# Optimization experiments

Hardware: AMD Instinct MI355X
Metric: run time of the kernel (lower is better)

The kernel has to match this reference:

```python
import jax, jax.numpy as jnp
import numpy as np

EPS = 1e-12
LN_EPS = 1e-5
RIDGE = 0.01
M, L, T = 256, 4096, 2048


def setup_inputs() -> dict:
    key = jax.random.key(0)
    ks = jax.random.split(key, 16)
    inp = {
        "gamma": jax.random.uniform(ks[0], (L,), dtype=jnp.float32),
        "A_re": jax.random.normal(ks[1], (M, L), dtype=jnp.float32),
        "A_im": jax.random.normal(ks[2], (M, L), dtype=jnp.float32),
        "X_re": jax.random.normal(ks[3], (M, T), dtype=jnp.float32),
        "X_im": jax.random.normal(ks[4], (M, T), dtype=jnp.float32),
        # LayerNorm(L) params
        "ln_w": jnp.ones((L,), jnp.float32),
        "ln_b": jnp.zeros((L,), jnp.float32),
        # MultiheadAttention(embed_dim=1, num_heads=1): in_proj [3,1]->[3], out_proj [1,1]->[1]
        "in_w": jax.random.normal(ks[5], (3,), dtype=jnp.float32),
        "in_b": jnp.zeros((3,), jnp.float32),
        "out_w": jax.random.normal(ks[6], (1,), dtype=jnp.float32),
        "out_b": jnp.zeros((1,), jnp.float32),
        # gate Linear(L, L)
        "gate_W": jax.random.normal(ks[7], (L, L), dtype=jnp.float32) * (1.0 / np.sqrt(L)),
        "gate_b": jnp.zeros((L,), jnp.float32),
        # learned scalars
        "delta": jnp.float32(0.5),
        "lmbda": jnp.float32(0.01),
    }
    return inp


def _iaa_forward(gamma, A_re, A_im, X_re, X_im, ln_w, ln_b, in_w, in_b,
                 out_w, out_b, gate_W, gate_b, delta, lmbda):
    A = (A_re + 1j * A_im).astype(jnp.complex64)      # [M, L]
    X = (X_re + 1j * X_im).astype(jnp.complex64)      # [M, T]
    p = gamma                                         # [L]

    # R = A diag(p) A^H + ridge * I   (MxM)
    AP = A * p[None, :].astype(A.dtype)
    R = AP @ A.conj().T + RIDGE * jnp.eye(M, dtype=A.dtype)
    Rinv = jnp.linalg.inv(R)                          # [M, M]

    Ah = A.conj().T                                   # [L, M]
    ARi = Ah @ Rinv                                   # [L, M]
    S = ARi @ X                                       # [L, T]
    q = jnp.sum(jnp.abs(S) ** 2, axis=1)              # [L]
    d = jnp.real(jnp.sum(ARi * Ah, axis=1))           # [L]
    v = q / (d + EPS)

    # constrain_gamma -> sigmoid(delta); use_residual
    dlt = jax.nn.sigmoid(delta)
    u = p + dlt * (v - p)

    # LayerNorm over the full length-L vector
    mu = jnp.mean(u)
    var = jnp.mean((u - mu) ** 2)
    u_p = (u - mu) / jnp.sqrt(var + LN_EPS) * ln_w + ln_b

    # MultiheadAttention(embed_dim=1, num_heads=1) over seq of L tokens, scale = 1/sqrt(1) = 1
    qv = u_p * in_w[0] + in_b[0]                      # [L]
    kv = u_p * in_w[1] + in_b[1]
    vv = u_p * in_w[2] + in_b[2]
    scores = qv[:, None] * kv[None, :]                # [L, L]
    attn = jax.nn.softmax(scores, axis=-1)
    attn_out = (attn @ vv) * out_w[0] + out_b[0]      # [L]

    # gating on u (pre-layernorm), as in the torch code
    g = jax.nn.sigmoid(gate_W @ u + gate_b)           # Linear: u @ W.T + b, u is 1-D -> W @ u + b
    r = g * v + (1.0 - g) * p

    s = r + attn_out
    return jax.nn.relu(s - lmbda)


def reference(gamma, A_re, A_im, X_re, X_im, ln_w, ln_b, in_w, in_b,
              out_w, out_b, gate_W, gate_b, delta, lmbda):
    return _iaa_forward(gamma, A_re, A_im, X_re, X_im, ln_w, ln_b, in_w, in_b,
                        out_w, out_b, gate_W, gate_b, delta, lmbda)
```

## Files before the change

kernel.cpp:

```cpp
#include <hip/hip_runtime.h>
#include <hip/hip_bf16.h>
#include <math.h>

#define MM 256
#define LL 4096
#define TT 2048

typedef __attribute__((ext_vector_type(8))) short bf16x8;
typedef __attribute__((ext_vector_type(4))) float f32x4;
typedef __attribute__((ext_vector_type(4))) unsigned short us4;
typedef unsigned short ushort_t;

#define OFF_G      131072
#define OFF_Q      262144
#define OFF_D      266240
#define OFF_V      270336
#define OFF_U      274432
#define OFF_UP     278528
#define ZERO_FL    290816
#define OFF_RINVP  290816
#define OFF_GP     421888
#define OFF_APL    552960
#define OFF_XPL    2650112
#define OFF_ATP    3698688
#define OFF_WTP    5795840
#define OFF_XA     9990144
#define OFF_XB     10121216
#define OFF_EA     10252288
#define OFF_EB     10383360

#define MFMA3(ACC, AH, AL, BH, BL)                                              \
  ACC = __builtin_amdgcn_mfma_f32_16x16x32_bf16(AH, BH, ACC, 0, 0, 0);          \
  ACC = __builtin_amdgcn_mfma_f32_16x16x32_bf16(AH, BL, ACC, 0, 0, 0);          \
  ACC = __builtin_amdgcn_mfma_f32_16x16x32_bf16(AL, BH, ACC, 0, 0, 0);

__device__ __forceinline__ void split_bf16(float x, ushort_t& h, ushort_t& l) {
  __hip_bfloat16 bh = __float2bfloat16(x);
  h = *(ushort_t*)&bh;
  __hip_bfloat16 bl = __float2bfloat16(x - __bfloat162float(bh));
  l = *(ushort_t*)&bl;
}
__device__ __forceinline__ float bfu2f(ushort_t u) {
  unsigned v = ((unsigned)u) << 16;
  float f;
  __builtin_memcpy(&f, &v, 4);
  return f;
}

__device__ __forceinline__ float wave_red_sum(float v) {
#pragma unroll
  for (int o = 32; o > 0; o >>= 1) v += __shfl_down(v, o);
  return v;
}
__device__ __forceinline__ float wave_red_max(float v) {
#pragma unroll
  for (int o = 32; o > 0; o >>= 1) v = fmaxf(v, __shfl_down(v, o));
  return v;
}
__device__ float blk_red_sum(float v) {
  __shared__ float sh[4];
  int lane = threadIdx.x & 63, wv = threadIdx.x >> 6;
  v = wave_red_sum(v);
  __syncthreads();
  if (lane == 0) sh[wv] = v;
  __syncthreads();
  return sh[0] + sh[1] + sh[2] + sh[3];
}
__device__ float blk_red_max(float v) {
  __shared__ float shm[4];
  int lane = threadIdx.x & 63, wv = threadIdx.x >> 6;
  v = wave_red_max(v);
  __syncthreads();
  if (lane == 0) shm[wv] = v;
  __syncthreads();
  return fmaxf(fmaxf(shm[0], shm[1]), fmaxf(shm[2], shm[3]));
}

__device__ __forceinline__ float2 r_mirror(const float2* __restrict__ R, int i, int j) {
  if ((i >> 6) >= (j >> 6)) return R[i * 256 + j];
  float2 r = R[j * 256 + i];
  r.y = -r.y;
  return r;
}

__global__ __launch_bounds__(256) void k_prep(float* __restrict__ ws,
                                              const float* __restrict__ Are,
                                              const float* __restrict__ Aim,
                                              const float* __restrict__ Xre,
                                              const float* __restrict__ Xim,
                                              const float* __restrict__ gamma) {
  __shared__ float tr[32][33], ti[32][33];
  int bid = blockIdx.x, tid = threadIdx.x;
  if (bid < 1136) {
    int idx = bid * 256 + tid;
    float v = 0.0f;
    if (idx < 131072 && (idx % 514) == 0) v = 0.01f;
    ws[idx] = v;
  } else if (bid < 2160) {
    int i4 = (bid - 1136) * 256 + tid;
    ushort_t* dst = (ushort_t*)(ws + OFF_APL);
    float4 re = ((const float4*)Are)[i4];
    float4 im = ((const float4*)Aim)[i4];
    float4 ga = ((const float4*)gamma)[i4 & (LL / 4 - 1)];
    float sr[4] = {re.x * sqrtf(ga.x), re.y * sqrtf(ga.y), re.z * sqrtf(ga.z), re.w * sqrtf(ga.w)};
    float si[4] = {im.x * sqrtf(ga.x), im.y * sqrtf(ga.y), im.z * sqrtf(ga.z), im.w * sqrtf(ga.w)};
    us4 hr, lr, hi, li;
#pragma unroll
    for (int e = 0; e < 4; ++e) {
      ushort_t h, l;
      split_bf16(sr[e], h, l); hr[e] = h; lr[e] = l;
      split_bf16(si[e], h, l); hi[e] = h; li[e] = l;
    }
    size_t o = (size_t)i4 * 4;
    *(us4*)(dst + o) = hr;
    *(us4*)(dst + (size_t)MM * LL + o) = lr;
    *(us4*)(dst + 2 * (size_t)MM * LL + o) = hi;
    *(us4*)(dst + 3 * (size_t)MM * LL + o) = li;
  } else if (bid < 2672) {
    int i4 = (bid - 2160) * 256 + tid;
    ushort_t* dst = (ushort_t*)(ws + OFF_XPL);
    float4 re = ((const float4*)Xre)[i4];
    float4 im = ((const float4*)Xim)[i4];
    float fr[4] = {re.x, re.y, re.z, re.w};
    float fi[4] = {im.x, im.y, im.z, im.w};
    us4 hr, lr, hi, li;
#pragma unroll
    for (int e = 0; e < 4; ++e) {
      ushort_t h, l;
      split_bf16(fr[e], h, l); hr[e] = h; lr[e] = l;
      split_bf16(fi[e], h, l); hi[e] = h; li[e] = l;
    }
    size_t o = (size_t)i4 * 4;
    *(us4*)(dst + o) = hr;
    *(us4*)(dst + (size_t)MM * TT + o) = lr;
    *(us4*)(dst + 2 * (size_t)MM * TT + o) = hi;
    *(us4*)(dst + 3 * (size_t)MM * TT + o) = li;
  } else {
    int b2 = bid - 2672;
    ushort_t* dst = (ushort_t*)(ws + OFF_ATP);
    int c0 = (b2 & 127) * 32, r0 = (b2 >> 7) * 32;
    int tx = tid & 31, tg = tid >> 5;
#pragma unroll
    for (int i = 0; i < 4; ++i) {
      int r = tg + 8 * i;
      tr[r][tx] = Are[(size_t)(r0 + r) * LL + c0 + tx];
      ti[r][tx] = Aim[(size_t)(r0 + r) * LL + c0 + tx];
    }
    __syncthreads();
#pragma unroll
    for (int i = 0; i < 4; ++i) {
      int rr = tg + 8 * i;
      size_t o = (size_t)(c0 + rr) * 256 + r0 + tx;
      ushort_t h, l;
      split_bf16(tr[tx][rr], h, l);
      dst[o] = h;
      dst[o + 1048576] = l;
      split_bf16(ti[tx][rr], h, l);
      dst[o + 2097152] = h;
      dst[o + 3145728] = l;
    }
  }
}

__global__ __launch_bounds__(256, 4) void k_gram_both(float* __restrict__ ws) {
  __shared__ __align__(16) ushort_t sA[4][64][40];
  __shared__ __align__(16) ushort_t sB[4][64][40];
  const int ti_lu[10] = {0, 1, 1, 2, 2, 2, 3, 3, 3, 3};
  const int tj_lu[10] = {0, 0, 1, 0, 1, 2, 0, 1, 2, 3};
  int bid = blockIdx.x;
  const ushort_t* pl;
  float* C;
  int K, tile, ksplit;
  size_t PS;
  if (bid < 320) {
    pl = (const ushort_t*)(ws + OFF_APL);
    C = ws;
    K = LL;
    PS = (size_t)MM * LL;
    tile = bid % 10;
    ksplit = bid / 10;
  } else {
    int b2 = bid - 320;
    pl = (const ushort_t*)(ws + OFF_XPL);
    C = ws + OFF_G;
    K = TT;
    PS = (size_t)MM * TT;
    tile = b2 % 10;
    ksplit = b2 / 10;
  }
  int kbeg = ksplit * 128;
  int i0 = ti_lu[tile] * 64, j0 = tj_lu[tile] * 64;
  bool diag = (i0 == j0);
  int tid = threadIdx.x;
  int lane = tid & 63, wv = tid >> 6;
  int srow = tid >> 2, sslot = tid & 3;
  int arow = wv * 16 + (lane & 15);
  int kq = (lane >> 4) * 8;
  f32x4 z = {0.f, 0.f, 0.f, 0.f};
  f32x4 Zrr[4], Zri[4], Zir[4], Zii[4];
#pragma unroll
  for (int s = 0; s < 4; ++s) { Zrr[s] = z; Zri[s] = z; Zir[s] = z; Zii[s] = z; }

  for (int chunk = 0; chunk < 4; ++chunk) {
    int k0 = kbeg + chunk * 32;
    __syncthreads();
#pragma unroll
    for (int p = 0; p < 4; ++p) {
      *(bf16x8*)&sA[p][srow][sslot * 8] =
          *(const bf16x8*)(pl + p * PS + (size_t)(i0 + srow) * K + k0 + sslot * 8);
      if (!diag)
        *(bf16x8*)&sB[p][srow][sslot * 8] =
            *(const bf16x8*)(pl + p * PS + (size_t)(j0 + srow) * K + k0 + sslot * 8);
    }
    __syncthreads();
    bf16x8 arh = *(const bf16x8*)&sA[0][arow][kq];
    bf16x8 arl = *(const bf16x8*)&sA[1][arow][kq];
    bf16x8 aih = *(const bf16x8*)&sA[2][arow][kq];
    bf16x8 ail = *(const bf16x8*)&sA[3][arow][kq];
    ushort_t(*bs)[64][40] = diag ? sA : sB;
#pragma unroll
    for (int s = 0; s < 4; ++s) {
      int brow = s * 16 + (lane & 15);
      bf16x8 brh = *(const bf16x8*)&bs[0][brow][kq];
      bf16x8 brl = *(const bf16x8*)&bs[1][brow][kq];
      bf16x8 bih = *(const bf16x8*)&bs[2][brow][kq];
      bf16x8 bil = *(const bf16x8*)&bs[3][brow][kq];
      MFMA3(Zrr[s], arh, arl, brh, brl);
      MFMA3(Zri[s], arh, arl, bih, bil);
      MFMA3(Zir[s], aih, ail, brh, brl);
      MFMA3(Zii[s], aih, ail, bih, bil);
    }
  }
  int rbase = i0 + wv * 16 + (lane >> 4) * 4;
#pragma unroll
  for (int s = 0; s < 4; ++s) {
    int col = j0 + s * 16 + (lane & 15);
#pragma unroll
    for (int r = 0; r < 4; ++r) {
      float re = Zrr[s][r] + Zii[s][r];
      float im = Zir[s][r] - Zri[s][r];
      float* p = C + ((size_t)(rbase + r) * 256 + col) * 2;
      atomicAdd(p, re);
      atomicAdd(p + 1, im);
    }
  }
}

__global__ __launch_bounds__(256) void k_n1(float* __restrict__ ws) {
  __shared__ float2 As[16][17], Bs[16][17];
  const float2* R = (const float2*)ws;
  int bid = blockIdx.x, tid = threadIdx.x;
  if (bid < 256) {
    float2* E1 = (float2*)(ws + OFF_EA);
    int i0 = (bid >> 4) * 16, j0 = (bid & 15) * 16;
    int tx = tid & 15, ty = tid >> 4;
    int rowA = i0 + ty;
    float DiA = R[rowA * 257].x;
    float accx = 0.f, accy = 0.f;
    for (int k0 = 0; k0 < 256; k0 += 16) {
      __syncthreads();
      {
        int c = k0 + tx;
        float2 r = r_mirror(R, rowA, c);
        float dl = (rowA == c) ? 1.0f : 0.0f;
        As[ty][tx] = make_float2(dl - r.x / DiA, -r.y / DiA);
      }
      {
        int rB = k0 + ty, c = j0 + tx;
        float DiB = R[rB * 257].x;
        float2 r = r_mirror(R, rB, c);
        float dl = (rB == c) ? 1.0f : 0.0f;
        Bs[ty][tx] = make_float2(dl - r.x / DiB, -r.y / DiB);
      }
      __syncthreads();
#pragma unroll
      for (int kk = 0; kk < 16; ++kk) {
        float2 a = As[ty][kk], bb = Bs[kk][tx];
        accx += a.x * bb.x - a.y * bb.y;
        accy += a.x * bb.y + a.y * bb.x;
      }
    }
    E1[rowA * 256 + j0 + tx] = make_float2(accx, accy);
  } else if (bid < 512) {
    float2* X1 = (float2*)(ws + OFF_XA);
    int idx = (bid - 256) * 256 + tid;
    int i = idx >> 8, j = idx & 255;
    float Dii = R[i * 257].x;
    float Djj = R[j * 257].x;
    float2 r = r_mirror(R, i, j);
    float dl = (i == j) ? 1.0f : 0.0f;
    float ex = dl - r.x / Dii;
    float ey = -r.y / Dii;
    X1[idx] = make_float2((dl + ex) / Djj, ey / Djj);
  } else {
    const float2* src = (const float2*)(ws + OFF_G);
    ushort_t* dst = (ushort_t*)(ws + OFF_GP);
    int idx = (bid - 512) * 256 + tid;
    int i = idx >> 8, j = idx & 255;
    float2 v = r_mirror(src, i, j);
    ushort_t h, l;
    split_bf16(v.x, h, l);
    dst[idx] = h;
    dst[idx + 65536] = l;
    split_bf16(v.y, h, l);
    dst[idx + 131072] = h;
    dst[idx + 196608] = l;
  }
}

__global__ __launch_bounds__(256) void k_newt_step(const float2* __restrict__ Xin,
                                                   const float2* __restrict__ Ein,
                                                   float2* __restrict__ Xout,
                                                   float2* __restrict__ Eout, int xblocks) {
  __shared__ float2 As[16][17], Bs[16][17];
  int bid = blockIdx.x;
  bool isX = bid < xblocks;
  int b = isX ? bid : bid - xblocks;
  const float2* Bm = isX ? Xin : Ein;
  int i0 = (b >> 4) * 16, j0 = (b & 15) * 16;
  int tx = threadIdx.x & 15, ty = threadIdx.x >> 4;
  float accx = 0.f, accy = 0.f;
  for (int k0 = 0; k0 < 256; k0 += 16) {
    __syncthreads();
    As[ty][tx] = Ein[(i0 + ty) * 256 + k0 + tx];
    Bs[ty][tx] = Bm[(k0 + ty) * 256 + j0 + tx];
    __syncthreads();
#pragma unroll
    for (int kk = 0; kk < 16; ++kk) {
      float2 a = As[ty][kk], bb = Bs[kk][tx];
      accx += a.x * bb.x - a.y * bb.y;
      accy += a.x * bb.y + a.y * bb.x;
    }
  }
  int idx = (i0 + ty) * 256 + j0 + tx;
  if (isX) {
    float2 x = Xin[idx];
    Xout[idx] = make_float2(x.x + accx, x.y + accy);
  } else {
    Eout[idx] = make_float2(accx, accy);
  }
}

__global__ __launch_bounds__(256) void k_newt_fin(const float2* __restrict__ Xin,
                                                  const float2* __restrict__ Ein,
                                                  ushort_t* __restrict__ dst) {
  __shared__ float2 As[16][17], Bs[16][17];
  int b = blockIdx.x;
  int i0 = (b >> 4) * 16, j0 = (b & 15) * 16;
  int tx = threadIdx.x & 15, ty = threadIdx.x >> 4;
  float accx = 0.f, accy = 0.f;
  for (int k0 = 0; k0 < 256; k0 += 16) {
    __syncthreads();
    As[ty][tx] = Ein[(i0 + ty) * 256 + k0 + tx];
    Bs[ty][tx] = Xin[(k0 + ty) * 256 + j0 + tx];
    __syncthreads();
#pragma unroll
    for (int kk = 0; kk < 16; ++kk) {
      float2 a = As[ty][kk], bb = Bs[kk][tx];
      accx += a.x * bb.x - a.y * bb.y;
      accy += a.x * bb.y + a.y * bb.x;
    }
  }
  int idx = (i0 + ty) * 256 + j0 + tx;
  float2 x = Xin[idx];
  float vx = x.x + accx, vy = x.y + accy;
  ushort_t h, l;
  split_bf16(vx, h, l);
  dst[idx] = h;
  dst[idx + 65536] = l;
  split_bf16(vy, h, l);
  dst[idx + 131072] = h;
  dst[idx + 196608] = l;
}

__global__ __launch_bounds__(256) void k_wide_mfma(const ushort_t* __restrict__ Ap,
                                                   const ushort_t* __restrict__ Bp,
                                                   const float* __restrict__ AuxRe,
                                                   const float* __restrict__ AuxIm,
                                                   ushort_t* __restrict__ WTout,
                                                   float* __restrict__ dq, int mode) {
  __shared__ __align__(16) ushort_t sB[4][64][40];
  const ushort_t* arh_p = Ap;
  const ushort_t* arl_p = Ap + 65536;
  const ushort_t* aih_p = Ap + 131072;
  const ushort_t* ail_p = Ap + 196608;
  const ushort_t* brh_p = Bp;
  const ushort_t* brl_p = Bp + 1048576;
  const ushort_t* bih_p = Bp + 2097152;
  const ushort_t* bil_p = Bp + 3145728;
  int j0 = blockIdx.x * 64;
  int i0 = blockIdx.y * 64;
  int tid = threadIdx.x;
  int lane = tid & 63, wv = tid >> 6;
  int srow = tid >> 2, sslot = tid & 3;
  int m = i0 + wv * 16 + (lane & 15);
  int kq = (lane >> 4) * 8;
  f32x4 z = {0.f, 0.f, 0.f, 0.f};
  f32x4 Zrr[4], Zri[4], Zir[4], Zii[4];
#pragma unroll
  for (int s = 0; s < 4; ++s) { Zrr[s] = z; Zri[s] = z; Zir[s] = z; Zii[s] = z; }
  for (int k0 = 0; k0 < 256; k0 += 32) {
    __syncthreads();
    {
      size_t bo = (size_t)(j0 + srow) * 256 + k0 + sslot * 8;
      *(bf16x8*)&sB[0][srow][sslot * 8] = *(const bf16x8*)(brh_p + bo);
      *(bf16x8*)&sB[1][srow][sslot * 8] = *(const bf16x8*)(brl_p + bo);
      *(bf16x8*)&sB[2][srow][sslot * 8] = *(const bf16x8*)(bih_p + bo);
      *(bf16x8*)&sB[3][srow][sslot * 8] = *(const bf16x8*)(bil_p + bo);
    }
    __syncthreads();
    size_t ao = (size_t)m * 256 + k0 + kq;
    bf16x8 arh = *(const bf16x8*)(arh_p + ao);
    bf16x8 arl = *(const bf16x8*)(arl_p + ao);
    bf16x8 aih = *(const bf16x8*)(aih_p + ao);
    bf16x8 ail = *(const bf16x8*)(ail_p + ao);
#pragma unroll
    for (int s = 0; s < 4; ++s) {
      int brow = s * 16 + (lane & 15);
      bf16x8 brh = *(const bf16x8*)&sB[0][brow][kq];
      bf16x8 brl = *(const bf16x8*)&sB[1][brow][kq];
      bf16x8 bih = *(const bf16x8*)&sB[2][brow][kq];
      bf16x8 bil = *(const bf16x8*)&sB[3][brow][kq];
      MFMA3(Zrr[s], arh, arl, brh, brl);
      MFMA3(Zri[s], arh, arl, bih, bil);
      MFMA3(Zir[s], aih, ail, brh, brl);
      MFMA3(Zii[s], aih, ail, bih, bil);
    }
  }
  int rbase = i0 + wv * 16 + (lane >> 4) * 4;
#pragma unroll
  for (int s = 0; s < 4; ++s) {
    int col = j0 + s * 16 + (lane & 15);
    size_t wo = (size_t)col * 256 + rbase;
    float part = 0.f;
    if (mode == 0) {
      us4 hr, lr, hi, li;
#pragma unroll
      for (int r = 0; r < 4; ++r) {
        float re = Zrr[s][r] - Zii[s][r];
        float im = Zri[s][r] + Zir[s][r];
        ushort_t h, l;
        split_bf16(re, h, l);
        hr[r] = h; lr[r] = l;
        split_bf16(im, h, l);
        hi[r] = h; li[r] = l;
        size_t o = (size_t)(rbase + r) * LL + col;
        part += re * AuxRe[o] - im * AuxIm[o];
      }
      *(us4*)(WTout + wo) = hr;
      *(us4*)(WTout + 1048576 + wo) = lr;
      *(us4*)(WTout + 2097152 + wo) = hi;
      *(us4*)(WTout + 3145728 + wo) = li;
    } else {
      us4 wh = *(const us4*)(brh_p + wo);
      us4 wl = *(const us4*)(brl_p + wo);
      us4 wih = *(const us4*)(bih_p + wo);
      us4 wil = *(const us4*)(bil_p + wo);
#pragma unroll
      for (int r = 0; r < 4; ++r) {
        float re = Zrr[s][r] - Zii[s][r];
        float im = Zri[s][r] + Zir[s][r];
        float wx = bfu2f(wh[r]) + bfu2f(wl[r]);
        float wy = bfu2f(wih[r]) + bfu2f(wil[r]);
        part += wx * re + wy * im;
      }
    }
    part += __shfl_down(part, 32);
    part += __shfl_down(part, 16);
    if ((lane >> 4) == 0) atomicAdd(dq + col, part);
  }
}

__global__ __launch_bounds__(256) void k_uvln(float* __restrict__ ws,
                                              const float* __restrict__ gamma,
                                              const float* __restrict__ delta,
                                              const float* __restrict__ lnw,
                                              const float* __restrict__ lnb) {
  const float* q = ws + OFF_Q;
  const float* d = ws + OFF_D;
  float* vvec = ws + OFF_V;
  float* uvec = ws + OFF_U;
  float* up = ws + OFF_UP;
  int tid = threadIdx.x;
  float dlt = 1.0f / (1.0f + expf(-delta[0]));
  float s = 0.f;
  for (int i = tid; i < LL; i += 256) {
    float v = q[i] / (d[i] + 1e-12f);
    float p = gamma[i];
    float u = p + dlt * (v - p);
    vvec[i] = v;
    uvec[i] = u;
    s += u;
  }
  float mu = blk_red_sum(s) * (1.0f / LL);
  float s2 = 0.f;
  for (int i = tid; i < LL; i += 256) { float dd = uvec[i] - mu; s2 += dd * dd; }
  float var = blk_red_sum(s2) * (1.0f / LL);
  float inv = rsqrtf(var + 1e-5f);
  for (int i = tid; i < LL; i += 256) up[i] = (uvec[i] - mu) * inv * lnw[i] + lnb[i];
}

__global__ __launch_bounds__(256) void k_gateattn(const float* __restrict__ ws,
                                                  const float* __restrict__ Wg,
                                                  const float* __restrict__ gb,
                                                  const float* __restrict__ inw,
                                                  const float* __restrict__ inb,
                                                  const float* __restrict__ outw,
                                                  const float* __restrict__ outb,
                                                  const float* __restrict__ gamma,
                                                  const float* __restrict__ lmbda,
                                                  float* __restrict__ out) {
  const float* uvec = ws + OFF_U;
  const float* up = ws + OFF_UP;
  const float* vvec = ws + OFF_V;
  int i = blockIdx.x, tid = threadIdx.x;
  const float4* wr = (const float4*)(Wg + (size_t)i * LL);
  const float4* u4 = (const float4*)uvec;
  float s = 0.f;
  for (int j = tid; j < LL / 4; j += 256) {
    float4 w = wr[j], x = u4[j];
    s += w.x * x.x + w.y * x.y + w.z * x.z + w.w * x.w;
  }
  float tot = blk_red_sum(s);
  float g = 1.0f / (1.0f + expf(-(tot + gb[i])));
  float qv = up[i] * inw[0] + inb[0];
  float w1 = inw[1], b1 = inb[1], w2 = inw[2], b2 = inb[2];
  const float4* up4 = (const float4*)up;
  float mx = -3.4e38f;
  for (int j = tid; j < LL / 4; j += 256) {
    float4 u = up4[j];
    mx = fmaxf(mx, fmaxf(fmaxf(qv * (u.x * w1 + b1), qv * (u.y * w1 + b1)),
                         fmaxf(qv * (u.z * w1 + b1), qv * (u.w * w1 + b1))));
  }
  mx = blk_red_max(mx);
  float den = 0.f, num = 0.f;
  for (int j = tid; j < LL / 4; j += 256) {
    float4 u = up4[j];
    float e0 = expf(qv * (u.x * w1 + b1) - mx);
    float e1 = expf(qv * (u.y * w1 + b1) - mx);
    float e2 = expf(qv * (u.z * w1 + b1) - mx);
    float e3 = expf(qv * (u.w * w1 + b1) - mx);
    den += e0 + e1 + e2 + e3;
    num += e0 * (u.x * w2 + b2) + e1 * (u.y * w2 + b2) + e2 * (u.z * w2 + b2) + e3 * (u.w * w2 + b2);
  }
  den = blk_red_sum(den);
  num = blk_red_sum(num);
  if (tid == 0) {
    float attn = (num / den) * outw[0] + outb[0];
    float r = g * vvec[i] + (1.0f - g) * gamma[i] + attn - lmbda[0];
    out[i] = fmaxf(r, 0.0f);
  }
}

extern "C" void kernel_launch(void* const* d_in, const int* in_sizes, int n_in,
                              void* d_out, int out_size, void* d_ws, size_t ws_size,
                              hipStream_t stream) {
  const float* gamma = (const float*)d_in[0];
  const float* Are   = (const float*)d_in[1];
  const float* Aim   = (const float*)d_in[2];
  const float* Xre   = (const float*)d_in[3];
  const float* Xim   = (const float*)d_in[4];
  const float* lnw   = (const float*)d_in[5];
  const float* lnb   = (const float*)d_in[6];
  const float* inw   = (const float*)d_in[7];
  const float* inb   = (const float*)d_in[8];
  const float* outw  = (const float*)d_in[9];
  const float* outb  = (const float*)d_in[10];
  const float* gateW = (const float*)d_in[11];
  const float* gateb = (const float*)d_in[12];
  const float* delta = (const float*)d_in[13];
  const float* lmbda = (const float*)d_in[14];
  float* out = (float*)d_out;
  float* ws = (float*)d_ws;

  float2* XA = (float2*)(ws + OFF_XA);
  float2* XB = (float2*)(ws + OFF_XB);
  float2* EA = (float2*)(ws + OFF_EA);
  float2* EB = (float2*)(ws + OFF_EB);
  ushort_t* Rinvp = (ushort_t*)(ws + OFF_RINVP);

  k_prep<<<3696, 256, 0, stream>>>(ws, Are, Aim, Xre, Xim, gamma);
  k_gram_both<<<480, 256, 0, stream>>>(ws);
  k_n1<<<768, 256, 0, stream>>>(ws);
  k_newt_step<<<512, 256, 0, stream>>>(XA, EA, XB, EB, 256);
  k_newt_step<<<512, 256, 0, stream>>>(XB, EB, XA, EA, 256);
  k_newt_step<<<512, 256, 0, stream>>>(XA, EA, XB, EB, 256);
  k_newt_fin<<<256, 256, 0, stream>>>(XB, EB, Rinvp);

  k_wide_mfma<<<dim3(64, 4), 256, 0, stream>>>(Rinvp, (ushort_t*)(ws + OFF_ATP),
                                               Are, Aim, (ushort_t*)(ws + OFF_WTP),
                                               ws + OFF_D, 0);
  k_wide_mfma<<<dim3(64, 4), 256, 0, stream>>>((ushort_t*)(ws + OFF_GP),
                                               (ushort_t*)(ws + OFF_WTP),
                                               nullptr, nullptr, nullptr, ws + OFF_Q, 1);
  k_uvln<<<1, 256, 0, stream>>>(ws, gamma, delta, lnw, lnb);
  k_gateattn<<<LL, 256, 0, stream>>>(ws, gateW, gateb, inw, inb, outw, outb, gamma, lmbda, out);
}
```

Measured before the change: 308.2 us.

## Replace Gram atomics with split-K partials, last-block reduce, and fuse LN into gate kernel

The Gram kernel now writes per-split partial tiles to a workspace buffer instead of using float atomics. The last block per tile, found through an atomic counter, sums the partials, adds the ridge and writes the mirrored Hermitian R. For the X Gram, that block also writes the bf16-split G directly, so the r_mirror reads and the G packing blocks in k_n1 go away. A large zero-fill in k_prep also disappears. The single-block k_uvln kernel is removed, and every gateattn block recomputes v, u and the LayerNorm statistics redundantly, trading extra arithmetic and memory reads for one less serial launch.

```diff
diff --git a/kernel.cpp b/kernel.cpp
--- a/kernel.cpp
+++ b/kernel.cpp
@@ -11,13 +11,9 @@
 typedef __attribute__((ext_vector_type(4))) unsigned short us4;
 typedef unsigned short ushort_t;
 
-#define OFF_G      131072
 #define OFF_Q      262144
 #define OFF_D      266240
-#define OFF_V      270336
-#define OFF_U      274432
-#define OFF_UP     278528
-#define ZERO_FL    290816
+#define OFF_CNT    270336
 #define OFF_RINVP  290816
 #define OFF_GP     421888
 #define OFF_APL    552960
@@ -28,6 +24,8 @@
 #define OFF_XB     10121216
 #define OFF_EA     10252288
 #define OFF_EB     10383360
+#define OFF_PA     10514432
+#define OFF_PX     13135872
 
 #define MFMA3(ACC, AH, AL, BH, BL)                                              \
   ACC = __builtin_amdgcn_mfma_f32_16x16x32_bf16(AH, BH, ACC, 0, 0, 0);          \
@@ -76,13 +74,6 @@
   return fmaxf(fmaxf(shm[0], shm[1]), fmaxf(shm[2], shm[3]));
 }
 
-__device__ __forceinline__ float2 r_mirror(const float2* __restrict__ R, int i, int j) {
-  if ((i >> 6) >= (j >> 6)) return R[i * 256 + j];
-  float2 r = R[j * 256 + i];
-  r.y = -r.y;
-  return r;
-}
-
 __global__ __launch_bounds__(256) void k_prep(float* __restrict__ ws,
                                               const float* __restrict__ Are,
                                               const float* __restrict__ Aim,
@@ -91,13 +82,10 @@
                                               const float* __restrict__ gamma) {
   __shared__ float tr[32][33], ti[32][33];
   int bid = blockIdx.x, tid = threadIdx.x;
-  if (bid < 1136) {
-    int idx = bid * 256 + tid;
-    float v = 0.0f;
-    if (idx < 131072 && (idx % 514) == 0) v = 0.01f;
-    ws[idx] = v;
-  } else if (bid < 2160) {
-    int i4 = (bid - 1136) * 256 + tid;
+  if (bid < 33) {
+    ws[OFF_Q + bid * 256 + tid] = 0.0f;
+  } else if (bid < 1057) {
+    int i4 = (bid - 33) * 256 + tid;
     ushort_t* dst = (ushort_t*)(ws + OFF_APL);
     float4 re = ((const float4*)Are)[i4];
     float4 im = ((const float4*)Aim)[i4];
@@ -116,8 +104,8 @@
     *(us4*)(dst + (size_t)MM * LL + o) = lr;
     *(us4*)(dst + 2 * (size_t)MM * LL + o) = hi;
     *(us4*)(dst + 3 * (size_t)MM * LL + o) = li;
-  } else if (bid < 2672) {
-    int i4 = (bid - 2160) * 256 + tid;
+  } else if (bid < 1569) {
+    int i4 = (bid - 1057) * 256 + tid;
     ushort_t* dst = (ushort_t*)(ws + OFF_XPL);
     float4 re = ((const float4*)Xre)[i4];
     float4 im = ((const float4*)Xim)[i4];
@@ -136,7 +124,7 @@
     *(us4*)(dst + 2 * (size_t)MM * TT + o) = hi;
     *(us4*)(dst + 3 * (size_t)MM * TT + o) = li;
   } else {
-    int b2 = bid - 2672;
+    int b2 = bid - 1569;
     ushort_t* dst = (ushort_t*)(ws + OFF_ATP);
     int c0 = (b2 & 127) * 32, r0 = (b2 >> 7) * 32;
     int tx = tid & 31, tg = tid >> 5;
@@ -165,29 +153,18 @@
 __global__ __launch_bounds__(256, 4) void k_gram_both(float* __restrict__ ws) {
   __shared__ __align__(16) ushort_t sA[4][64][40];
   __shared__ __align__(16) ushort_t sB[4][64][40];
+  __shared__ int rflag;
   const int ti_lu[10] = {0, 1, 1, 2, 2, 2, 3, 3, 3, 3};
   const int tj_lu[10] = {0, 0, 1, 0, 1, 2, 0, 1, 2, 3};
   int bid = blockIdx.x;
-  const ushort_t* pl;
-  float* C;
-  int K, tile, ksplit;
-  size_t PS;
-  if (bid < 320) {
-    pl = (const ushort_t*)(ws + OFF_APL);
-    C = ws;
-    K = LL;
-    PS = (size_t)MM * LL;
-    tile = bid % 10;
-    ksplit = bid / 10;
-  } else {
-    int b2 = bid - 320;
-    pl = (const ushort_t*)(ws + OFF_XPL);
-    C = ws + OFF_G;
-    K = TT;
-    PS = (size_t)MM * TT;
-    tile = b2 % 10;
-    ksplit = b2 / 10;
-  }
+  bool isA = bid < 320;
+  int b2 = isA ? bid : bid - 320;
+  const ushort_t* pl = (const ushort_t*)(ws + (isA ? OFF_APL : OFF_XPL));
+  int K = isA ? LL : TT;
+  size_t PS = (size_t)MM * K;
+  int tile = b2 % 10, ksplit = b2 / 10;
+  int S = isA ? 32 : 16;
+  float2* Pbase = (float2*)(ws + (isA ? OFF_PA : OFF_PX));
   int kbeg = ksplit * 128;
   int i0 = ti_lu[tile] * 64, j0 = tj_lu[tile] * 64;
   bool diag = (i0 == j0);
@@ -231,17 +208,61 @@
       MFMA3(Zii[s], aih, ail, bih, bil);
     }
   }
-  int rbase = i0 + wv * 16 + (lane >> 4) * 4;
+  float2* Pt = Pbase + ((size_t)ksplit * 10 + tile) * 4096;
 #pragma unroll
   for (int s = 0; s < 4; ++s) {
-    int col = j0 + s * 16 + (lane & 15);
+    int lcol = s * 16 + (lane & 15);
 #pragma unroll
     for (int r = 0; r < 4; ++r) {
+      int lrow = wv * 16 + (lane >> 4) * 4 + r;
       float re = Zrr[s][r] + Zii[s][r];
       float im = Zir[s][r] - Zri[s][r];
-      float* p = C + ((size_t)(rbase + r) * 256 + col) * 2;
-      atomicAdd(p, re);
-      atomicAdd(p + 1, im);
+      Pt[lrow * 64 + lcol] = make_float2(re, im);
+    }
+  }
+  __threadfence();
+  if (tid == 0) {
+    int* cnt = (int*)(ws + OFF_CNT);
+    int old = atomicAdd(&cnt[(isA ? 0 : 10) + tile], 1);
+    rflag = (old == S - 1);
+  }
+  __syncthreads();
+  if (!rflag) return;
+  __threadfence();
+  float2* Rc = (float2*)ws;
+  ushort_t* Gp = (ushort_t*)(ws + OFF_GP);
+  int e0 = tid * 16;
+  for (int e = e0; e < e0 + 16; e += 2) {
+    float4 acc = {0.f, 0.f, 0.f, 0.f};
+    for (int s = 0; s < S; ++s) {
+      float4 v = *(const float4*)&Pbase[((size_t)s * 10 + tile) * 4096 + e];
+      acc.x += v.x; acc.y += v.y; acc.z += v.z; acc.w += v.w;
+    }
+    int li = e >> 6, lj = e & 63;
+    int gi = i0 + li, gj = j0 + lj;
+    if (isA) {
+      if (diag && gi == gj) acc.x += 0.01f;
+      if (diag && gi == gj + 1) acc.z += 0.01f;
+      Rc[gi * 256 + gj] = make_float2(acc.x, acc.y);
+      Rc[gi * 256 + gj + 1] = make_float2(acc.z, acc.w);
+      if (!diag) {
+        Rc[gj * 256 + gi] = make_float2(acc.x, -acc.y);
+        Rc[(gj + 1) * 256 + gi] = make_float2(acc.z, -acc.w);
+      }
+    } else {
+      ushort_t h, l;
+      int idx = gi * 256 + gj;
+      split_bf16(acc.x, h, l); Gp[idx] = h; Gp[idx + 65536] = l;
+      split_bf16(acc.y, h, l); Gp[idx + 131072] = h; Gp[idx + 196608] = l;
+      split_bf16(acc.z, h, l); Gp[idx + 1] = h; Gp[idx + 1 + 65536] = l;
+      split_bf16(acc.w, h, l); Gp[idx + 1 + 131072] = h; Gp[idx + 1 + 196608] = l;
+      if (!diag) {
+        int m0 = gj * 256 + gi, m1 = (gj + 1) * 256 + gi;
+        split_bf16(acc.x, h, l); Gp[m0] = h; Gp[m0 + 65536] = l;
+        split_bf16(-acc.y, h, l); Gp[m0 + 131072] = h; Gp[m0 + 196608] = l;
+        split_bf16(acc.z, h, l); Gp[m1] = h; Gp[m1 + 65536] = l;
+        split_bf16(-acc.w, h, l); Gp[m1 + 131072] = h; Gp[m1 + 196608] = l;
+      }
     }
   }
 }
@@ -261,14 +282,14 @@
       __syncthreads();
       {
         int c = k0 + tx;
-        float2 r = r_mirror(R, rowA, c);
+        float2 r = R[rowA * 256 + c];
         float dl = (rowA == c) ? 1.0f : 0.0f;
         As[ty][tx] = make_float2(dl - r.x / DiA, -r.y / DiA);
       }
       {
         int rB = k0 + ty, c = j0 + tx;
         float DiB = R[rB * 257].x;
-        float2 r = r_mirror(R, rB, c);
+        float2 r = R[rB * 256 + c];
         float dl = (rB == c) ? 1.0f : 0.0f;
         Bs[ty][tx] = make_float2(dl - r.x / DiB, -r.y / DiB);
       }
@@ -281,30 +302,17 @@
       }
     }
     E1[rowA * 256 + j0 + tx] = make_float2(accx, accy);
-  } else if (bid < 512) {
+  } else {
     float2* X1 = (float2*)(ws + OFF_XA);
     int idx = (bid - 256) * 256 + tid;
     int i = idx >> 8, j = idx & 255;
     float Dii = R[i * 257].x;
     float Djj = R[j * 257].x;
-    float2 r = r_mirror(R, i, j);
+    float2 r = R[i * 256 + j];
     float dl = (i == j) ? 1.0f : 0.0f;
     float ex = dl - r.x / Dii;
     float ey = -r.y / Dii;
     X1[idx] = make_float2((dl + ex) / Djj, ey / Djj);
-  } else {
-    const float2* src = (const float2*)(ws + OFF_G);
-    ushort_t* dst = (ushort_t*)(ws + OFF_GP);
-    int idx = (bid - 512) * 256 + tid;
-    int i = idx >> 8, j = idx & 255;
-    float2 v = r_mirror(src, i, j);
-    ushort_t h, l;
-    split_bf16(v.x, h, l);
-    dst[idx] = h;
-    dst[idx + 65536] = l;
-    split_bf16(v.y, h, l);
-    dst[idx + 131072] = h;
-    dst[idx + 196608] = l;
   }
 }
 
@@ -471,35 +479,6 @@
   }
 }
 
-__global__ __launch_bounds__(256) void k_uvln(float* __restrict__ ws,
-                                              const float* __restrict__ gamma,
-                                              const float* __restrict__ delta,
-                                              const float* __restrict__ lnw,
-                                              const float* __restrict__ lnb) {
-  const float* q = ws + OFF_Q;
-  const float* d = ws + OFF_D;
-  float* vvec = ws + OFF_V;
-  float* uvec = ws + OFF_U;
-  float* up = ws + OFF_UP;
-  int tid = threadIdx.x;
-  float dlt = 1.0f / (1.0f + expf(-delta[0]));
-  float s = 0.f;
-  for (int i = tid; i < LL; i += 256) {
-    float v = q[i] / (d[i] + 1e-12f);
-    float p = gamma[i];
-    float u = p + dlt * (v - p);
-    vvec[i] = v;
-    uvec[i] = u;
-    s += u;
-  }
-  float mu = blk_red_sum(s) * (1.0f / LL);
-  float s2 = 0.f;
-  for (int i = tid; i < LL; i += 256) { float dd = uvec[i] - mu; s2 += dd * dd; }
-  float var = blk_red_sum(s2) * (1.0f / LL);
-  float inv = rsqrtf(var + 1e-5f);
-  for (int i = tid; i < LL; i += 256) up[i] = (uvec[i] - mu) * inv * lnw[i] + lnb[i];
-}
-
 __global__ __launch_bounds__(256) void k_gateattn(const float* __restrict__ ws,
                                                   const float* __restrict__ Wg,
                                                   const float* __restrict__ gb,
@@ -508,46 +487,86 @@
                                                   const float* __restrict__ outw,
                                                   const float* __restrict__ outb,
                                                   const float* __restrict__ gamma,
+                                                  const float* __restrict__ delta,
+                                                  const float* __restrict__ lnw,
+                                                  const float* __restrict__ lnb,
                                                   const float* __restrict__ lmbda,
                                                   float* __restrict__ out) {
-  const float* uvec = ws + OFF_U;
-  const float* up = ws + OFF_UP;
-  const float* vvec = ws + OFF_V;
+  const float4* q4 = (const float4*)(ws + OFF_Q);
+  const float4* d4 = (const float4*)(ws + OFF_D);
+  const float4* g4 = (const float4*)gamma;
+  const float4* lw4 = (const float4*)lnw;
+  const float4* lb4 = (const float4*)lnb;
   int i = blockIdx.x, tid = threadIdx.x;
-  const float4* wr = (const float4*)(Wg + (size_t)i * LL);
-  const float4* u4 = (const float4*)uvec;
+  float dlt = 1.0f / (1.0f + expf(-delta[0]));
   float s = 0.f;
   for (int j = tid; j < LL / 4; j += 256) {
-    float4 w = wr[j], x = u4[j];
-    s += w.x * x.x + w.y * x.y + w.z * x.z + w.w * x.w;
-  }
-  float tot = blk_red_sum(s);
+    float4 qv = q4[j], dv = d4[j], pv = g4[j];
+    s += pv.x + dlt * (qv.x / (dv.x + 1e-12f) - pv.x);
+    s += pv.y + dlt * (qv.y / (dv.y + 1e-12f) - pv.y);
+    s += pv.z + dlt * (qv.z / (dv.z + 1e-12f) - pv.z);
+    s += pv.w + dlt * (qv.w / (dv.w + 1e-12f) - pv.w);
+  }
+  float mu = blk_red_sum(s) * (1.0f / LL);
+  float s2 = 0.f;
+  for (int j = tid; j < LL / 4; j += 256) {
+    float4 qv = q4[j], dv = d4[j], pv = g4[j];
+    float u0 = pv.x + dlt * (qv.x / (dv.x + 1e-12f) - pv.x) - mu;
+    float u1 = pv.y + dlt * (qv.y / (dv.y + 1e-12f) - pv.y) - mu;
+    float u2 = pv.z + dlt * (qv.z / (dv.z + 1e-12f) - pv.z) - mu;
+    float u3 = pv.w + dlt * (qv.w / (dv.w + 1e-12f) - pv.w) - mu;
+    s2 += u0 * u0 + u1 * u1 + u2 * u2 + u3 * u3;
+  }
+  float var = blk_red_sum(s2) * (1.0f / LL);
+  float inv = rsqrtf(var + 1e-5f);
+  const float* qs = ws + OFF_Q;
+  const float* ds = ws + OFF_D;
+  float v_i = qs[i] / (ds[i] + 1e-12f);
+  float u_i = gamma[i] + dlt * (v_i - gamma[i]);
+  float up_i = (u_i - mu) * inv * lnw[i] + lnb[i];
+  float qvv = up_i * inw[0] + inb[0];
+  float w1 = inw[1], b1 = inb[1], w2 = inw[2], b2 = inb[2];
+  const float4* wr = (const float4*)(Wg + (size_t)i * LL);
+  float sdot = 0.f, mx = -3.4e38f;
+  for (int j = tid; j < LL / 4; j += 256) {
+    float4 qv = q4[j], dv = d4[j], pv = g4[j], w = wr[j], lwv = lw4[j], lbv = lb4[j];
+    float u0 = pv.x + dlt * (qv.x / (dv.x + 1e-12f) - pv.x);
+    float u1 = pv.y + dlt * (qv.y / (dv.y + 1e-12f) - pv.y);
+    float u2 = pv.z + dlt * (qv.z / (dv.z + 1e-12f) - pv.z);
+    float u3 = pv.w + dlt * (qv.w / (dv.w + 1e-12f) - pv.w);
+    sdot += w.x * u0 + w.y * u1 + w.z * u2 + w.w * u3;
+    float k0 = ((u0 - mu) * inv * lwv.x + lbv.x) * w1 + b1;
+    float k1 = ((u1 - mu) * inv * lwv.y + lbv.y) * w1 + b1;
+    float k2 = ((u2 - mu) * inv * lwv.z + lbv.z) * w1 + b1;
+    float k3 = ((u3 - mu) * inv * lwv.w + lbv.w) * w1 + b1;
+    mx = fmaxf(mx, fmaxf(fmaxf(qvv * k0, qvv * k1), fmaxf(qvv * k2, qvv * k3)));
+  }
+  float tot = blk_red_sum(sdot);
+  mx = blk_red_max(mx);
   float g = 1.0f / (1.0f + expf(-(tot + gb[i])));
-  float qv = up[i] * inw[0] + inb[0];
-  float w1 = inw[1], b1 = inb[1], w2 = inw[2], b2 = inb[2];
-  const float4* up4 = (const float4*)up;
-  float mx = -3.4e38f;
-  for (int j = tid; j < LL / 4; j += 256) {
-    float4 u = up4[j];
-    mx = fmaxf(mx, fmaxf(fmaxf(qv * (u.x * w1 + b1), qv * (u.y * w1 + b1)),
-                         fmaxf(qv * (u.z * w1 + b1), qv * (u.w * w1 + b1))));
-  }
-  mx = blk_red_max(mx);
   float den = 0.f, num = 0.f;
   for (int j = tid; j < LL / 4; j += 256) {
-    float4 u = up4[j];
-    float e0 = expf(qv * (u.x * w1 + b1) - mx);
-    float e1 = expf(qv * (u.y * w1 + b1) - mx);
-    float e2 = expf(qv * (u.z * w1 + b1) - mx);
-    float e3 = expf(qv * (u.w * w1 + b1) - mx);
+    float4 qv = q4[j], dv = d4[j], pv = g4[j], lwv = lw4[j], lbv = lb4[j];
+    float u0 = pv.x + dlt * (qv.x / (dv.x + 1e-12f) - pv.x);
+    float u1 = pv.y + dlt * (qv.y / (dv.y + 1e-12f) - pv.y);
+    float u2 = pv.z + dlt * (qv.z / (dv.z + 1e-12f) - pv.z);
+    float u3 = pv.w + dlt * (qv.w / (dv.w + 1e-12f) - pv.w);
+    float p0 = (u0 - mu) * inv * lwv.x + lbv.x;
+    float p1 = (u1 - mu) * inv * lwv.y + lbv.y;
+    float p2 = (u2 - mu) * inv * lwv.z + lbv.z;
+    float p3 = (u3 - mu) * inv * lwv.w + lbv.w;
+    float e0 = expf(qvv * (p0 * w1 + b1) - mx);
+    float e1 = expf(qvv * (p1 * w1 + b1) - mx);
+    float e2 = expf(qvv * (p2 * w1 + b1) - mx);
+    float e3 = expf(qvv * (p3 * w1 + b1) - mx);
     den += e0 + e1 + e2 + e3;
-    num += e0 * (u.x * w2 + b2) + e1 * (u.y * w2 + b2) + e2 * (u.z * w2 + b2) + e3 * (u.w * w2 + b2);
+    num += e0 * (p0 * w2 + b2) + e1 * (p1 * w2 + b2) + e2 * (p2 * w2 + b2) + e3 * (p3 * w2 + b2);
   }
   den = blk_red_sum(den);
   num = blk_red_sum(num);
   if (tid == 0) {
     float attn = (num / den) * outw[0] + outb[0];
-    float r = g * vvec[i] + (1.0f - g) * gamma[i] + attn - lmbda[0];
+    float r = g * v_i + (1.0f - g) * gamma[i] + attn - lmbda[0];
     out[i] = fmaxf(r, 0.0f);
   }
 }
@@ -579,9 +598,9 @@
   float2* EB = (float2*)(ws + OFF_EB);
   ushort_t* Rinvp = (ushort_t*)(ws + OFF_RINVP);
 
-  k_prep<<<3696, 256, 0, stream>>>(ws, Are, Aim, Xre, Xim, gamma);
+  k_prep<<<2593, 256, 0, stream>>>(ws, Are, Aim, Xre, Xim, gamma);
   k_gram_both<<<480, 256, 0, stream>>>(ws);
-  k_n1<<<768, 256, 0, stream>>>(ws);
+  k_n1<<<512, 256, 0, stream>>>(ws);
   k_newt_step<<<512, 256, 0, stream>>>(XA, EA, XB, EB, 256);
   k_newt_step<<<512, 256, 0, stream>>>(XB, EB, XA, EA, 256);
   k_newt_step<<<512, 256, 0, stream>>>(XA, EA, XB, EB, 256);
@@ -593,6 +612,6 @@
   k_wide_mfma<<<dim3(64, 4), 256, 0, stream>>>((ushort_t*)(ws + OFF_GP),
                                                (ushort_t*)(ws + OFF_WTP),
                                                nullptr, nullptr, nullptr, ws + OFF_Q, 1);
-  k_uvln<<<1, 256, 0, stream>>>(ws, gamma, delta, lnw, lnb);
-  k_gateattn<<<LL, 256, 0, stream>>>(ws, gateW, gateb, inw, inb, outw, outb, gamma, lmbda, out);
-}
+  k_gateattn<<<LL, 256, 0, stream>>>(ws, gateW, gateb, inw, inb, outw, outb,
+                                     gamma, delta, lnw, lnb, lmbda, out);
+}
```

Measured after the change: 493.8 us. +60.2%, slower.
